# Optimization experiments

Hardware: AMD Instinct MI355X
Metric: run time of the kernel (lower is better)

The kernel has to match this reference:

```python
import jax, jax.numpy as jnp
import numpy as np
from jax import lax

N_LAYER = 24
N_EMBD = 1024
FFN = 4 * N_EMBD
LN_EPS = 1e-5


def setup_inputs() -> dict:
    key = jax.random.key(0)
    ks = jax.random.split(key, 24)
    L, C, F = N_LAYER, N_EMBD, FFN
    s = C ** -0.5  # keep GEMV outputs O(1) so exp() stays finite

    def rn(k, shape, scale=1.0):
        return jax.random.normal(k, shape, dtype=jnp.float32) * scale

    state = jnp.concatenate([
        rn(ks[1], (1, L, C)),                                          # statea: prev ln1 output
        rn(ks[2], (1, L, C), 0.1),                                     # stateb: wkv numerator acc
        jax.random.uniform(ks[3], (1, L, C), dtype=jnp.float32) + 0.5, # statec: wkv denominator acc (>0)
        rn(ks[4], (1, L, C)),                                          # stated: prev ln2 output
    ], axis=0)

    return {
        "x": rn(ks[0], (C,)),
        "state": state,
        "ln1w": 1.0 + rn(ks[5], (L, C), 0.02),
        "ln1b": rn(ks[6], (L, C), 0.02),
        "ln2w": 1.0 + rn(ks[7], (L, C), 0.02),
        "ln2b": rn(ks[8], (L, C), 0.02),
        "time_decay": -jnp.abs(rn(ks[9], (L, C))) - 0.1,
        "time_first": rn(ks[10], (L, C), 0.1),
        "kktk": jax.random.uniform(ks[11], (L, C), dtype=jnp.float32),
        "vvtv": jax.random.uniform(ks[12], (L, C), dtype=jnp.float32),
        "rrtr": jax.random.uniform(ks[13], (L, C), dtype=jnp.float32),
        "key": rn(ks[14], (L, 3, C, C), s),        # [kk, vv, -rr] stacks
        "outputv": rn(ks[15], (L, C, C), s),
        "time_mix_k_ffn": jax.random.uniform(ks[16], (L, C), dtype=jnp.float32),
        "time_mix_r_ffn": jax.random.uniform(ks[17], (L, C), dtype=jnp.float32),
        "key_ffn": rn(ks[18], (L, F, C), s),
        "receptance_ffn": rn(ks[19], (L, C, C), s),  # stored pre-negated, as in the module
        "value_ffn": rn(ks[20], (L, C, F), F ** -0.5),
    }


def _ln(v, w, b):
    m = v.mean()
    var = ((v - m) ** 2).mean()
    return (v - m) * lax.rsqrt(var + LN_EPS) * w + b


def reference(x, state, ln1w, ln1b, ln2w, ln2b, time_decay, time_first,
              kktk, vvtv, rrtr, key, outputv, time_mix_k_ffn, time_mix_r_ffn,
              key_ffn, receptance_ffn, value_ffn):
    # offset = 0, so the state slice covers all layers
    statea, stateb, statec, stated = state[0], state[1], state[2], state[3]  # each [L, C]
    # token-shift contributions precomputed against previous-step state
    kk_s = kktk * statea
    vv_s = vvtv * statea
    rr_s = rrtr * statea
    tmk_s = time_mix_k_ffn * stated
    tmr_s = time_mix_r_ffn * stated

    def layer(xc, p):
        (l1w, l1b, l2w, l2b, td, tfst, kks, vvs, rrs, keym, outv,
         tmk, tmr, kffn, rffn, vffn, sb, sc) = p
        xy = _ln(xc, l1w, l1b)
        k = keym[0] @ (xy + kks)
        v = keym[1] @ (xy + vvs)
        r = keym[2] @ (xy + rrs)   # keym[2] holds -receptance weights
        etfk = jnp.exp(tfst + k)
        w = (sb + etfk * v) / (sc * jnp.exp(r) + jnp.exp(tfst + k + r) + sc + etfk)
        sxx = xc + outv @ w
        ek = jnp.exp(k)
        ed = jnp.exp(td)
        sb_new = sb * ed + ek * v
        sc_new = sc * ed + ek
        xx = _ln(sxx, l2w, l2b)
        kf = jnp.square(jax.nn.relu(kffn @ (xx + tmk)))
        rf = jnp.exp(rffn @ (xx + tmr))  # rffn already negated
        x_new = sxx + (vffn @ kf) / (rf + 1.0)
        return x_new, (xy, sb_new, sc_new, xx)

    xs = (ln1w, ln1b, ln2w, ln2b, time_decay, time_first, kk_s, vv_s, rr_s,
          key, outputv, tmk_s, tmr_s, key_ffn, receptance_ffn, value_ffn,
          stateb, statec)
    x_out, (sa_n, sb_n, sc_n, sd_n) = lax.scan(layer, x, xs)
    new_state = jnp.stack([sa_n, sb_n, sc_n, sd_n])  # [4, L, C]
    return x_out, new_state
```

## Files before the change

kernel.cpp:

```cpp
#include <hip/hip_runtime.h>
#include <math.h>
#include <stddef.h>

#define NLAYER 24
#define NEMBD  1024
#define NFFN   4096
#define NB     256
#define NT     256
#define NW     4
#define LN_EPS 1e-5f

#define OUT_SA (NEMBD)
#define OUT_SB (NEMBD + NLAYER*NEMBD)
#define OUT_SC (NEMBD + 2*NLAYER*NEMBD)
#define OUT_SD (NEMBD + 3*NLAYER*NEMBD)

#define FLAG_STRIDE 32

struct Params {
  const float *x, *state, *ln1w, *ln1b, *ln2w, *ln2b, *td, *tf, *kktk, *vvtv, *rrtr;
  const float *key, *outputv, *tmk, *tmr, *kffn, *rffn, *vffn;
  float *out;
  float *xbuf, *kvr, *sxx, *rfb, *kfb;
  unsigned *flags;
};

__device__ __forceinline__ float wred(float v) {
#pragma unroll
  for (int o = 32; o > 0; o >>= 1) v += __shfl_xor(v, o, 64);
  return v;
}

__device__ __forceinline__ float dot4(float4 a, float4 b) {
  return a.x*b.x + a.y*b.y + a.z*b.z + a.w*b.w;
}

__device__ __forceinline__ float gload(const float* a) {
  return __hip_atomic_load(a, __ATOMIC_RELAXED, __HIP_MEMORY_SCOPE_AGENT);
}
__device__ __forceinline__ void gstore(float* a, float v) {
  __hip_atomic_store(a, v, __ATOMIC_RELAXED, __HIP_MEMORY_SCOPE_AGENT);
}

__device__ __forceinline__ void bar_arrive(unsigned* flags, unsigned tgt) {
  __syncthreads();
  asm volatile("" ::: "memory");
  if (threadIdx.x == 0) {
    __hip_atomic_store(&flags[(unsigned)blockIdx.x * FLAG_STRIDE], tgt,
                       __ATOMIC_RELAXED, __HIP_MEMORY_SCOPE_AGENT);
  }
  asm volatile("" ::: "memory");
}

__device__ __forceinline__ void bar_wait(unsigned* flags, unsigned tgt) {
  asm volatile("" ::: "memory");
  long spin = 0;
  while (__hip_atomic_load(&flags[(unsigned)threadIdx.x * FLAG_STRIDE],
                           __ATOMIC_RELAXED, __HIP_MEMORY_SCOPE_AGENT) < tgt) {
    __builtin_amdgcn_s_sleep(1);
    if (++spin > (1L << 18)) break;
  }
  asm volatile("" ::: "memory");
  __syncthreads();
}

__global__ void __launch_bounds__(NT, 1)
rwkv_persistent(Params p) {
  const int b    = blockIdx.x;
  const int t    = threadIdx.x;
  const int wid  = t >> 6;
  const int lane = t & 63;

  __shared__ float lds[NFFN];
  __shared__ float reda[NW], redq[NW];
  __shared__ float mrs[2];

  float4 wr[20];
  unsigned g = 1;

  {
    const float* W = p.key + (size_t)(b * 12 + wid * 3) * NEMBD + lane * 4;
#pragma unroll
    for (int r = 0; r < 3; ++r)
#pragma unroll
      for (int jj = 0; jj < 4; ++jj)
        wr[r * 4 + jj] = *(const float4*)&W[(size_t)r * NEMBD + jj * 256];
  }

  for (int l = 0; l < NLAYER; ++l) {
    {
      const int i0 = t * 4;
      float xa[4];
      if (l == 0) {
        float4 x4 = *(const float4*)&p.x[i0];
        xa[0] = x4.x; xa[1] = x4.y; xa[2] = x4.z; xa[3] = x4.w;
      } else {
#pragma unroll
        for (int j = 0; j < 4; ++j) xa[j] = gload(&p.xbuf[i0 + j]);
      }
      float s = xa[0] + xa[1] + xa[2] + xa[3];
      float q = xa[0]*xa[0] + xa[1]*xa[1] + xa[2]*xa[2] + xa[3]*xa[3];
      s = wred(s); q = wred(q);
      if (lane == 0) { reda[wid] = s; redq[wid] = q; }
      __syncthreads();
      if (t == 0) {
        float ts = 0.f, tq = 0.f;
#pragma unroll
        for (int i = 0; i < NW; ++i) { ts += reda[i]; tq += redq[i]; }
        float m = ts * (1.f / NEMBD);
        float var = tq * (1.f / NEMBD) - m * m;
        mrs[0] = m; mrs[1] = rsqrtf(var + LN_EPS);
      }
      __syncthreads();
      float m = mrs[0], rs = mrs[1];
      const float* l1w = p.ln1w + l * NEMBD;
      const float* l1b = p.ln1b + l * NEMBD;
      const float* sa  = p.state + 0 * NLAYER * NEMBD + l * NEMBD;
      const float* kkp = p.kktk + l * NEMBD;
      const float* vvp = p.vvtv + l * NEMBD;
      const float* rrp = p.rrtr + l * NEMBD;
#pragma unroll
      for (int j = 0; j < 4; ++j) {
        int i = i0 + j;
        float xy = (xa[j] - m) * rs * l1w[i] + l1b[i];
        float sav = sa[i];
        lds[i]             = xy + kkp[i] * sav;
        lds[NEMBD + i]     = xy + vvp[i] * sav;
        lds[2 * NEMBD + i] = xy + rrp[i] * sav;
        if (b == 0) p.out[OUT_SA + l * NEMBD + i] = xy;
      }
      __syncthreads();

      const int r0 = b * 12 + wid * 3;
      const float* v0 = lds + ((r0 + 0) >> 10) * NEMBD;
      const float* v1 = lds + ((r0 + 1) >> 10) * NEMBD;
      const float* v2 = lds + ((r0 + 2) >> 10) * NEMBD;
      float a0 = 0.f, a1 = 0.f, a2 = 0.f;
#pragma unroll
      for (int jj = 0; jj < 4; ++jj) {
        int col = lane * 4 + jj * 256;
        a0 += dot4(wr[0 * 4 + jj], *(const float4*)&v0[col]);
        a1 += dot4(wr[1 * 4 + jj], *(const float4*)&v1[col]);
        a2 += dot4(wr[2 * 4 + jj], *(const float4*)&v2[col]);
      }
      a0 = wred(a0); a1 = wred(a1); a2 = wred(a2);
      if (lane == 0) {
        gstore(&p.kvr[r0 + 0], a0);
        gstore(&p.kvr[r0 + 1], a1);
        gstore(&p.kvr[r0 + 2], a2);
      }
    }
    bar_arrive(p.flags, g);
    const int row2 = b * 4 + wid;
    {
      const float* W = p.outputv + ((size_t)l * NEMBD + row2) * NEMBD + lane * 4;
#pragma unroll
      for (int jj = 0; jj < 4; ++jj)
        wr[jj] = *(const float4*)&W[jj * 256];
    }
    bar_wait(p.flags, g); ++g;

    {
      const int i0 = t * 4;
      const float* tfp = p.tf + l * NEMBD;
      const float* sbp = p.state + 1 * NLAYER * NEMBD + l * NEMBD;
      const float* scp = p.state + 2 * NLAYER * NEMBD + l * NEMBD;
      const float* tdp = p.td + l * NEMBD;
#pragma unroll
      for (int j = 0; j < 4; ++j) {
        int i = i0 + j;
        float k = gload(&p.kvr[i]);
        float v = gload(&p.kvr[NEMBD + i]);
        float r = gload(&p.kvr[2 * NEMBD + i]);
        float sb = sbp[i], sc = scp[i];
        float etfk = expf(tfp[i] + k);
        float er   = expf(r);
        lds[i] = (sb + etfk * v) / ((sc + etfk) * (1.f + er));
        if (b == 0) {
          float ek = expf(k), ed = expf(tdp[i]);
          p.out[OUT_SB + l * NEMBD + i] = sb * ed + ek * v;
          p.out[OUT_SC + l * NEMBD + i] = sc * ed + ek;
        }
      }
      __syncthreads();
      float acc = 0.f;
#pragma unroll
      for (int jj = 0; jj < 4; ++jj) {
        int col = lane * 4 + jj * 256;
        acc += dot4(wr[jj], *(const float4*)&lds[col]);
      }
      acc = wred(acc);
      if (lane == 0) {
        float xc = (l == 0) ? p.x[row2] : gload(&p.xbuf[row2]);
        gstore(&p.sxx[row2], xc + acc);
      }
    }
    bar_arrive(p.flags, g);
    int isk3[5], rid3[5], voff3[5];
    {
#pragma unroll
      for (int sI = 0; sI < 5; ++sI) {
        int qI = wid * 5 + sI;
        const float* wp;
        if (qI < 16) {
          int row = b * 16 + qI;
          wp = p.kffn + ((size_t)l * NFFN + row) * NEMBD;
          isk3[sI] = 1; rid3[sI] = row; voff3[sI] = 0;
        } else {
          int row = b * 4 + (qI - 16);
          wp = p.rffn + ((size_t)l * NEMBD + row) * NEMBD;
          isk3[sI] = 0; rid3[sI] = row; voff3[sI] = NEMBD;
        }
        wp += lane * 4;
#pragma unroll
        for (int jj = 0; jj < 4; ++jj)
          wr[sI * 4 + jj] = *(const float4*)&wp[jj * 256];
      }
    }
    bar_wait(p.flags, g); ++g;

    {
      const int i0 = t * 4;
      float xa[4];
#pragma unroll
      for (int j = 0; j < 4; ++j) xa[j] = gload(&p.sxx[i0 + j]);
      float s = xa[0] + xa[1] + xa[2] + xa[3];
      float q = xa[0]*xa[0] + xa[1]*xa[1] + xa[2]*xa[2] + xa[3]*xa[3];
      s = wred(s); q = wred(q);
      if (lane == 0) { reda[wid] = s; redq[wid] = q; }
      __syncthreads();
      if (t == 0) {
        float ts = 0.f, tq = 0.f;
#pragma unroll
        for (int i = 0; i < NW; ++i) { ts += reda[i]; tq += redq[i]; }
        float m = ts * (1.f / NEMBD);
        float var = tq * (1.f / NEMBD) - m * m;
        mrs[0] = m; mrs[1] = rsqrtf(var + LN_EPS);
      }
      __syncthreads();
      float m = mrs[0], rs = mrs[1];
      const float* l2w = p.ln2w + l * NEMBD;
      const float* l2b = p.ln2b + l * NEMBD;
      const float* sdp = p.state + 3 * NLAYER * NEMBD + l * NEMBD;
      const float* tmkp = p.tmk + l * NEMBD;
      const float* tmrp = p.tmr + l * NEMBD;
#pragma unroll
      for (int j = 0; j < 4; ++j) {
        int i = i0 + j;
        float xx = (xa[j] - m) * rs * l2w[i] + l2b[i];
        float sdv = sdp[i];
        lds[i]         = xx + tmkp[i] * sdv;
        lds[NEMBD + i] = xx + tmrp[i] * sdv;
        if (b == 0) p.out[OUT_SD + l * NEMBD + i] = xx;
      }
      __syncthreads();

      float acc[5] = {0.f, 0.f, 0.f, 0.f, 0.f};
#pragma unroll
      for (int jj = 0; jj < 4; ++jj) {
        int col = lane * 4 + jj * 256;
#pragma unroll
        for (int sI = 0; sI < 5; ++sI)
          acc[sI] += dot4(wr[sI * 4 + jj], *(const float4*)&lds[voff3[sI] + col]);
      }
#pragma unroll
      for (int sI = 0; sI < 5; ++sI) {
        float r = wred(acc[sI]);
        if (lane == 0) {
          if (isk3[sI]) { float kv = fmaxf(r, 0.f); gstore(&p.kfb[rid3[sI]], kv * kv); }
          else          { gstore(&p.rfb[rid3[sI]], expf(r)); }
        }
      }
    }
    bar_arrive(p.flags, g);
    const int row4 = b * 4 + wid;
    {
      const float* W = p.vffn + ((size_t)l * NEMBD + row4) * NFFN + lane * 4;
#pragma unroll
      for (int jj = 0; jj < 16; ++jj)
        wr[jj] = *(const float4*)&W[jj * 256];
    }
    bar_wait(p.flags, g); ++g;

    {
#pragma unroll
      for (int pass = 0; pass < 4; ++pass) {
        int idx = pass * NEMBD + t * 4;
        float a0 = gload(&p.kfb[idx + 0]);
        float a1 = gload(&p.kfb[idx + 1]);
        float a2 = gload(&p.kfb[idx + 2]);
        float a3 = gload(&p.kfb[idx + 3]);
        *(float4*)&lds[idx] = make_float4(a0, a1, a2, a3);
      }
      __syncthreads();
      float accA = 0.f, accB = 0.f;
#pragma unroll
      for (int jj = 0; jj < 16; jj += 2) {
        int col = lane * 4 + jj * 256;
        accA += dot4(wr[jj],     *(const float4*)&lds[col]);
        accB += dot4(wr[jj + 1], *(const float4*)&lds[col + 256]);
      }
      float acc = wred(accA + accB);
      if (lane == 0) {
        float xn = gload(&p.sxx[row4]) + acc / (gload(&p.rfb[row4]) + 1.f);
        if (l == NLAYER - 1) p.out[row4] = xn;
        else                 gstore(&p.xbuf[row4], xn);
      }
    }
    bar_arrive(p.flags, g);
    if (l < NLAYER - 1) {
      const float* W = p.key + (size_t)(l + 1) * 3 * NEMBD * NEMBD
                     + (size_t)(b * 12 + wid * 3) * NEMBD + lane * 4;
#pragma unroll
      for (int r = 0; r < 3; ++r)
#pragma unroll
        for (int jj = 0; jj < 4; ++jj)
          wr[r * 4 + jj] = *(const float4*)&W[(size_t)r * NEMBD + jj * 256];
    }
    bar_wait(p.flags, g); ++g;
  }
}

__global__ void rwkv_init(unsigned* flags) {
  flags[threadIdx.x * FLAG_STRIDE] = 0u;
}

extern "C" void kernel_launch(void* const* d_in, const int* in_sizes, int n_in,
                              void* d_out, int out_size, void* d_ws, size_t ws_size,
                              hipStream_t stream) {
  Params p;
  p.x       = (const float*)d_in[0];
  p.state   = (const float*)d_in[1];
  p.ln1w    = (const float*)d_in[2];
  p.ln1b    = (const float*)d_in[3];
  p.ln2w    = (const float*)d_in[4];
  p.ln2b    = (const float*)d_in[5];
  p.td      = (const float*)d_in[6];
  p.tf      = (const float*)d_in[7];
  p.kktk    = (const float*)d_in[8];
  p.vvtv    = (const float*)d_in[9];
  p.rrtr    = (const float*)d_in[10];
  p.key     = (const float*)d_in[11];
  p.outputv = (const float*)d_in[12];
  p.tmk     = (const float*)d_in[13];
  p.tmr     = (const float*)d_in[14];
  p.kffn    = (const float*)d_in[15];
  p.rffn    = (const float*)d_in[16];
  p.vffn    = (const float*)d_in[17];
  p.out     = (float*)d_out;

  float* ws = (float*)d_ws;
  p.xbuf = ws;
  p.kvr  = ws + NEMBD;
  p.sxx  = ws + 4 * NEMBD;
  p.rfb  = ws + 5 * NEMBD;
  p.kfb  = ws + 6 * NEMBD;
  p.flags = (unsigned*)((char*)d_ws + 49152);

  rwkv_init<<<1, NB, 0, stream>>>(p.flags);
  rwkv_persistent<<<NB, NT, 0, stream>>>(p);
}
```

Before: 534.8 us.

## Add dedicated polling wavefront for grid barrier and skip final-layer barrier

```diff
diff --git a/kernel.cpp b/kernel.cpp
--- a/kernel.cpp
+++ b/kernel.cpp
@@ -6,8 +6,8 @@
 #define NEMBD  1024
 #define NFFN   4096
 #define NB     256
-#define NT     256
-#define NW     4
+#define NT     320
+#define NWC    4
 #define LN_EPS 1e-5f
 
 #define OUT_SA (NEMBD)
@@ -42,43 +42,63 @@
   __hip_atomic_store(a, v, __ATOMIC_RELAXED, __HIP_MEMORY_SCOPE_AGENT);
 }
 
-__device__ __forceinline__ void bar_arrive(unsigned* flags, unsigned tgt) {
+__device__ __forceinline__ void bar_flag(unsigned* flags, unsigned tgt) {
   __syncthreads();
-  asm volatile("" ::: "memory");
   if (threadIdx.x == 0) {
     __hip_atomic_store(&flags[(unsigned)blockIdx.x * FLAG_STRIDE], tgt,
                        __ATOMIC_RELAXED, __HIP_MEMORY_SCOPE_AGENT);
   }
-  asm volatile("" ::: "memory");
-}
-
-__device__ __forceinline__ void bar_wait(unsigned* flags, unsigned tgt) {
-  asm volatile("" ::: "memory");
-  long spin = 0;
-  while (__hip_atomic_load(&flags[(unsigned)threadIdx.x * FLAG_STRIDE],
-                           __ATOMIC_RELAXED, __HIP_MEMORY_SCOPE_AGENT) < tgt) {
-    __builtin_amdgcn_s_sleep(1);
-    if (++spin > (1L << 18)) break;
+}
+
+__device__ __forceinline__ void bar_spin(unsigned* flags, unsigned tgt, unsigned* genw) {
+  const int wid  = threadIdx.x >> 6;
+  const int lane = threadIdx.x & 63;
+  if (wid == NWC) {
+    long spin = 0;
+    for (;;) {
+      bool mine = true;
+#pragma unroll
+      for (int j = 0; j < 4; ++j) {
+        unsigned f = __hip_atomic_load(&flags[(unsigned)(lane * 4 + j) * FLAG_STRIDE],
+                                       __ATOMIC_RELAXED, __HIP_MEMORY_SCOPE_AGENT);
+        mine &= (f >= tgt);
+      }
+      if (__all(mine)) break;
+      __builtin_amdgcn_s_sleep(1);
+      if (++spin > (1L << 18)) break;
+    }
+    if (lane == 0) {
+      __hip_atomic_store(genw, tgt, __ATOMIC_RELAXED, __HIP_MEMORY_SCOPE_WORKGROUP);
+    }
+  } else {
+    long spin = 0;
+    while (__hip_atomic_load(genw, __ATOMIC_RELAXED, __HIP_MEMORY_SCOPE_WORKGROUP) < tgt) {
+      __builtin_amdgcn_s_sleep(1);
+      if (++spin > (1L << 20)) break;
+    }
   }
-  asm volatile("" ::: "memory");
-  __syncthreads();
-}
-
-__global__ void __launch_bounds__(NT, 1)
+}
+
+__global__ void __launch_bounds__(NT, 2)
 rwkv_persistent(Params p) {
   const int b    = blockIdx.x;
   const int t    = threadIdx.x;
   const int wid  = t >> 6;
   const int lane = t & 63;
+  const bool cw  = (wid < NWC);
 
   __shared__ float lds[NFFN];
-  __shared__ float reda[NW], redq[NW];
+  __shared__ float reda[NWC], redq[NWC];
   __shared__ float mrs[2];
+  __shared__ unsigned genw;
+
+  if (t == 0) genw = 0u;
+  __syncthreads();
 
   float4 wr[20];
   unsigned g = 1;
 
-  {
+  if (cw) {
     const float* W = p.key + (size_t)(b * 12 + wid * 3) * NEMBD + lane * 4;
 #pragma unroll
     for (int r = 0; r < 3; ++r)
@@ -90,114 +110,123 @@
   for (int l = 0; l < NLAYER; ++l) {
     {
       const int i0 = t * 4;
-      float xa[4];
-      if (l == 0) {
-        float4 x4 = *(const float4*)&p.x[i0];
-        xa[0] = x4.x; xa[1] = x4.y; xa[2] = x4.z; xa[3] = x4.w;
-      } else {
-#pragma unroll
-        for (int j = 0; j < 4; ++j) xa[j] = gload(&p.xbuf[i0 + j]);
-      }
-      float s = xa[0] + xa[1] + xa[2] + xa[3];
-      float q = xa[0]*xa[0] + xa[1]*xa[1] + xa[2]*xa[2] + xa[3]*xa[3];
-      s = wred(s); q = wred(q);
-      if (lane == 0) { reda[wid] = s; redq[wid] = q; }
+      float xa[4] = {0.f, 0.f, 0.f, 0.f};
+      if (cw) {
+        if (l == 0) {
+          float4 x4 = *(const float4*)&p.x[i0];
+          xa[0] = x4.x; xa[1] = x4.y; xa[2] = x4.z; xa[3] = x4.w;
+        } else {
+#pragma unroll
+          for (int j = 0; j < 4; ++j) xa[j] = gload(&p.xbuf[i0 + j]);
+        }
+        float s = xa[0] + xa[1] + xa[2] + xa[3];
+        float q = xa[0]*xa[0] + xa[1]*xa[1] + xa[2]*xa[2] + xa[3]*xa[3];
+        s = wred(s); q = wred(q);
+        if (lane == 0) { reda[wid] = s; redq[wid] = q; }
+      }
       __syncthreads();
       if (t == 0) {
         float ts = 0.f, tq = 0.f;
 #pragma unroll
-        for (int i = 0; i < NW; ++i) { ts += reda[i]; tq += redq[i]; }
+        for (int i = 0; i < NWC; ++i) { ts += reda[i]; tq += redq[i]; }
         float m = ts * (1.f / NEMBD);
         float var = tq * (1.f / NEMBD) - m * m;
         mrs[0] = m; mrs[1] = rsqrtf(var + LN_EPS);
       }
       __syncthreads();
-      float m = mrs[0], rs = mrs[1];
-      const float* l1w = p.ln1w + l * NEMBD;
-      const float* l1b = p.ln1b + l * NEMBD;
-      const float* sa  = p.state + 0 * NLAYER * NEMBD + l * NEMBD;
-      const float* kkp = p.kktk + l * NEMBD;
-      const float* vvp = p.vvtv + l * NEMBD;
-      const float* rrp = p.rrtr + l * NEMBD;
-#pragma unroll
-      for (int j = 0; j < 4; ++j) {
-        int i = i0 + j;
-        float xy = (xa[j] - m) * rs * l1w[i] + l1b[i];
-        float sav = sa[i];
-        lds[i]             = xy + kkp[i] * sav;
-        lds[NEMBD + i]     = xy + vvp[i] * sav;
-        lds[2 * NEMBD + i] = xy + rrp[i] * sav;
-        if (b == 0) p.out[OUT_SA + l * NEMBD + i] = xy;
-      }
-      __syncthreads();
-
-      const int r0 = b * 12 + wid * 3;
-      const float* v0 = lds + ((r0 + 0) >> 10) * NEMBD;
-      const float* v1 = lds + ((r0 + 1) >> 10) * NEMBD;
-      const float* v2 = lds + ((r0 + 2) >> 10) * NEMBD;
-      float a0 = 0.f, a1 = 0.f, a2 = 0.f;
-#pragma unroll
-      for (int jj = 0; jj < 4; ++jj) {
-        int col = lane * 4 + jj * 256;
-        a0 += dot4(wr[0 * 4 + jj], *(const float4*)&v0[col]);
-        a1 += dot4(wr[1 * 4 + jj], *(const float4*)&v1[col]);
-        a2 += dot4(wr[2 * 4 + jj], *(const float4*)&v2[col]);
-      }
-      a0 = wred(a0); a1 = wred(a1); a2 = wred(a2);
-      if (lane == 0) {
-        gstore(&p.kvr[r0 + 0], a0);
-        gstore(&p.kvr[r0 + 1], a1);
-        gstore(&p.kvr[r0 + 2], a2);
-      }
-    }
-    bar_arrive(p.flags, g);
+      if (cw) {
+        float m = mrs[0], rs = mrs[1];
+        const float* l1w = p.ln1w + l * NEMBD;
+        const float* l1b = p.ln1b + l * NEMBD;
+        const float* sa  = p.state + 0 * NLAYER * NEMBD + l * NEMBD;
+        const float* kkp = p.kktk + l * NEMBD;
+        const float* vvp = p.vvtv + l * NEMBD;
+        const float* rrp = p.rrtr + l * NEMBD;
+#pragma unroll
+        for (int j = 0; j < 4; ++j) {
+          int i = i0 + j;
+          float xy = (xa[j] - m) * rs * l1w[i] + l1b[i];
+          float sav = sa[i];
+          lds[i]             = xy + kkp[i] * sav;
+          lds[NEMBD + i]     = xy + vvp[i] * sav;
+          lds[2 * NEMBD + i] = xy + rrp[i] * sav;
+          if (b == 0) p.out[OUT_SA + l * NEMBD + i] = xy;
+        }
+      }
+      __syncthreads();
+      if (cw) {
+        const int r0 = b * 12 + wid * 3;
+        const float* v0 = lds + ((r0 + 0) >> 10) * NEMBD;
+        const float* v1 = lds + ((r0 + 1) >> 10) * NEMBD;
+        const float* v2 = lds + ((r0 + 2) >> 10) * NEMBD;
+        float a0 = 0.f, a1 = 0.f, a2 = 0.f;
+#pragma unroll
+        for (int jj = 0; jj < 4; ++jj) {
+          int col = lane * 4 + jj * 256;
+          a0 += dot4(wr[0 * 4 + jj], *(const float4*)&v0[col]);
+          a1 += dot4(wr[1 * 4 + jj], *(const float4*)&v1[col]);
+          a2 += dot4(wr[2 * 4 + jj], *(const float4*)&v2[col]);
+        }
+        a0 = wred(a0); a1 = wred(a1); a2 = wred(a2);
+        if (lane == 0) {
+          gstore(&p.kvr[r0 + 0], a0);
+          gstore(&p.kvr[r0 + 1], a1);
+          gstore(&p.kvr[r0 + 2], a2);
+        }
+      }
+    }
+    bar_flag(p.flags, g);
     const int row2 = b * 4 + wid;
-    {
+    if (cw) {
       const float* W = p.outputv + ((size_t)l * NEMBD + row2) * NEMBD + lane * 4;
 #pragma unroll
       for (int jj = 0; jj < 4; ++jj)
         wr[jj] = *(const float4*)&W[jj * 256];
     }
-    bar_wait(p.flags, g); ++g;
+    bar_spin(p.flags, g, &genw); ++g;
 
     {
       const int i0 = t * 4;
-      const float* tfp = p.tf + l * NEMBD;
-      const float* sbp = p.state + 1 * NLAYER * NEMBD + l * NEMBD;
-      const float* scp = p.state + 2 * NLAYER * NEMBD + l * NEMBD;
-      const float* tdp = p.td + l * NEMBD;
-#pragma unroll
-      for (int j = 0; j < 4; ++j) {
-        int i = i0 + j;
-        float k = gload(&p.kvr[i]);
-        float v = gload(&p.kvr[NEMBD + i]);
-        float r = gload(&p.kvr[2 * NEMBD + i]);
-        float sb = sbp[i], sc = scp[i];
-        float etfk = expf(tfp[i] + k);
-        float er   = expf(r);
-        lds[i] = (sb + etfk * v) / ((sc + etfk) * (1.f + er));
-        if (b == 0) {
-          float ek = expf(k), ed = expf(tdp[i]);
-          p.out[OUT_SB + l * NEMBD + i] = sb * ed + ek * v;
-          p.out[OUT_SC + l * NEMBD + i] = sc * ed + ek;
-        }
-      }
-      __syncthreads();
-      float acc = 0.f;
-#pragma unroll
-      for (int jj = 0; jj < 4; ++jj) {
-        int col = lane * 4 + jj * 256;
-        acc += dot4(wr[jj], *(const float4*)&lds[col]);
-      }
-      acc = wred(acc);
-      if (lane == 0) {
-        float xc = (l == 0) ? p.x[row2] : gload(&p.xbuf[row2]);
-        gstore(&p.sxx[row2], xc + acc);
-      }
-    }
-    bar_arrive(p.flags, g);
+      if (cw) {
+        const float* tfp = p.tf + l * NEMBD;
+        const float* sbp = p.state + 1 * NLAYER * NEMBD + l * NEMBD;
+        const float* scp = p.state + 2 * NLAYER * NEMBD + l * NEMBD;
+        const float* tdp = p.td + l * NEMBD;
+#pragma unroll
+        for (int j = 0; j < 4; ++j) {
+          int i = i0 + j;
+          float k = gload(&p.kvr[i]);
+          float v = gload(&p.kvr[NEMBD + i]);
+          float r = gload(&p.kvr[2 * NEMBD + i]);
+          float sb = sbp[i], sc = scp[i];
+          float etfk = expf(tfp[i] + k);
+          float er   = expf(r);
+          lds[i] = (sb + etfk * v) / ((sc + etfk) * (1.f + er));
+          if (b == 0) {
+            float ek = expf(k), ed = expf(tdp[i]);
+            p.out[OUT_SB + l * NEMBD + i] = sb * ed + ek * v;
+            p.out[OUT_SC + l * NEMBD + i] = sc * ed + ek;
+          }
+        }
+      }
+      __syncthreads();
+      if (cw) {
+        float acc = 0.f;
+#pragma unroll
+        for (int jj = 0; jj < 4; ++jj) {
+          int col = lane * 4 + jj * 256;
+          acc += dot4(wr[jj], *(const float4*)&lds[col]);
+        }
+        acc = wred(acc);
+        if (lane == 0) {
+          float xc = (l == 0) ? p.x[row2] : gload(&p.xbuf[row2]);
+          gstore(&p.sxx[row2], xc + acc);
+        }
+      }
+    }
+    bar_flag(p.flags, g);
     int isk3[5], rid3[5], voff3[5];
-    {
+    if (cw) {
 #pragma unroll
       for (int sI = 0; sI < 5; ++sI) {
         int qI = wid * 5 + sI;
@@ -217,107 +246,118 @@
           wr[sI * 4 + jj] = *(const float4*)&wp[jj * 256];
       }
     }
-    bar_wait(p.flags, g); ++g;
+    bar_spin(p.flags, g, &genw); ++g;
 
     {
       const int i0 = t * 4;
-      float xa[4];
-#pragma unroll
-      for (int j = 0; j < 4; ++j) xa[j] = gload(&p.sxx[i0 + j]);
-      float s = xa[0] + xa[1] + xa[2] + xa[3];
-      float q = xa[0]*xa[0] + xa[1]*xa[1] + xa[2]*xa[2] + xa[3]*xa[3];
-      s = wred(s); q = wred(q);
-      if (lane == 0) { reda[wid] = s; redq[wid] = q; }
+      float xa[4] = {0.f, 0.f, 0.f, 0.f};
+      if (cw) {
+#pragma unroll
+        for (int j = 0; j < 4; ++j) xa[j] = gload(&p.sxx[i0 + j]);
+        float s = xa[0] + xa[1] + xa[2] + xa[3];
+        float q = xa[0]*xa[0] + xa[1]*xa[1] + xa[2]*xa[2] + xa[3]*xa[3];
+        s = wred(s); q = wred(q);
+        if (lane == 0) { reda[wid] = s; redq[wid] = q; }
+      }
       __syncthreads();
       if (t == 0) {
         float ts = 0.f, tq = 0.f;
 #pragma unroll
-        for (int i = 0; i < NW; ++i) { ts += reda[i]; tq += redq[i]; }
+        for (int i = 0; i < NWC; ++i) { ts += reda[i]; tq += redq[i]; }
         float m = ts * (1.f / NEMBD);
         float var = tq * (1.f / NEMBD) - m * m;
         mrs[0] = m; mrs[1] = rsqrtf(var + LN_EPS);
       }
       __syncthreads();
-      float m = mrs[0], rs = mrs[1];
-      const float* l2w = p.ln2w + l * NEMBD;
-      const float* l2b = p.ln2b + l * NEMBD;
-      const float* sdp = p.state + 3 * NLAYER * NEMBD + l * NEMBD;
-      const float* tmkp = p.tmk + l * NEMBD;
-      const float* tmrp = p.tmr + l * NEMBD;
-#pragma unroll
-      for (int j = 0; j < 4; ++j) {
-        int i = i0 + j;
-        float xx = (xa[j] - m) * rs * l2w[i] + l2b[i];
-        float sdv = sdp[i];
-        lds[i]         = xx + tmkp[i] * sdv;
-        lds[NEMBD + i] = xx + tmrp[i] * sdv;
-        if (b == 0) p.out[OUT_SD + l * NEMBD + i] = xx;
-      }
-      __syncthreads();
-
-      float acc[5] = {0.f, 0.f, 0.f, 0.f, 0.f};
-#pragma unroll
-      for (int jj = 0; jj < 4; ++jj) {
-        int col = lane * 4 + jj * 256;
-#pragma unroll
-        for (int sI = 0; sI < 5; ++sI)
-          acc[sI] += dot4(wr[sI * 4 + jj], *(const float4*)&lds[voff3[sI] + col]);
-      }
-#pragma unroll
-      for (int sI = 0; sI < 5; ++sI) {
-        float r = wred(acc[sI]);
-        if (lane == 0) {
-          if (isk3[sI]) { float kv = fmaxf(r, 0.f); gstore(&p.kfb[rid3[sI]], kv * kv); }
-          else          { gstore(&p.rfb[rid3[sI]], expf(r)); }
-        }
-      }
-    }
-    bar_arrive(p.flags, g);
+      if (cw) {
+        float m = mrs[0], rs = mrs[1];
+        const float* l2w = p.ln2w + l * NEMBD;
+        const float* l2b = p.ln2b + l * NEMBD;
+        const float* sdp = p.state + 3 * NLAYER * NEMBD + l * NEMBD;
+        const float* tmkp = p.tmk + l * NEMBD;
+        const float* tmrp = p.tmr + l * NEMBD;
+#pragma unroll
+        for (int j = 0; j < 4; ++j) {
+          int i = i0 + j;
+          float xx = (xa[j] - m) * rs * l2w[i] + l2b[i];
+          float sdv = sdp[i];
+          lds[i]         = xx + tmkp[i] * sdv;
+          lds[NEMBD + i] = xx + tmrp[i] * sdv;
+          if (b == 0) p.out[OUT_SD + l * NEMBD + i] = xx;
+        }
+      }
+      __syncthreads();
+      if (cw) {
+        float acc[5] = {0.f, 0.f, 0.f, 0.f, 0.f};
+#pragma unroll
+        for (int jj = 0; jj < 4; ++jj) {
+          int col = lane * 4 + jj * 256;
+#pragma unroll
+          for (int sI = 0; sI < 5; ++sI)
+            acc[sI] += dot4(wr[sI * 4 + jj], *(const float4*)&lds[voff3[sI] + col]);
+        }
+#pragma unroll
+        for (int sI = 0; sI < 5; ++sI) {
+          float r = wred(acc[sI]);
+          if (lane == 0) {
+            if (isk3[sI]) { float kv = fmaxf(r, 0.f); gstore(&p.kfb[rid3[sI]], kv * kv); }
+            else          { gstore(&p.rfb[rid3[sI]], expf(r)); }
+          }
+        }
+      }
+    }
+    bar_flag(p.flags, g);
     const int row4 = b * 4 + wid;
-    {
+    if (cw) {
       const float* W = p.vffn + ((size_t)l * NEMBD + row4) * NFFN + lane * 4;
 #pragma unroll
       for (int jj = 0; jj < 16; ++jj)
         wr[jj] = *(const float4*)&W[jj * 256];
     }
-    bar_wait(p.flags, g); ++g;
+    bar_spin(p.flags, g, &genw); ++g;
 
     {
-#pragma unroll
-      for (int pass = 0; pass < 4; ++pass) {
-        int idx = pass * NEMBD + t * 4;
-        float a0 = gload(&p.kfb[idx + 0]);
-        float a1 = gload(&p.kfb[idx + 1]);
-        float a2 = gload(&p.kfb[idx + 2]);
-        float a3 = gload(&p.kfb[idx + 3]);
-        *(float4*)&lds[idx] = make_float4(a0, a1, a2, a3);
-      }
-      __syncthreads();
-      float accA = 0.f, accB = 0.f;
-#pragma unroll
-      for (int jj = 0; jj < 16; jj += 2) {
-        int col = lane * 4 + jj * 256;
-        accA += dot4(wr[jj],     *(const float4*)&lds[col]);
-        accB += dot4(wr[jj + 1], *(const float4*)&lds[col + 256]);
-      }
-      float acc = wred(accA + accB);
-      if (lane == 0) {
-        float xn = gload(&p.sxx[row4]) + acc / (gload(&p.rfb[row4]) + 1.f);
-        if (l == NLAYER - 1) p.out[row4] = xn;
-        else                 gstore(&p.xbuf[row4], xn);
-      }
-    }
-    bar_arrive(p.flags, g);
+      if (cw) {
+#pragma unroll
+        for (int pass = 0; pass < 4; ++pass) {
+          int idx = pass * NEMBD + t * 4;
+          float a0 = gload(&p.kfb[idx + 0]);
+          float a1 = gload(&p.kfb[idx + 1]);
+          float a2 = gload(&p.kfb[idx + 2]);
+          float a3 = gload(&p.kfb[idx + 3]);
+          *(float4*)&lds[idx] = make_float4(a0, a1, a2, a3);
+        }
+      }
+      __syncthreads();
+      if (cw) {
+        float accA = 0.f, accB = 0.f;
+#pragma unroll
+        for (int jj = 0; jj < 16; jj += 2) {
+          int col = lane * 4 + jj * 256;
+          accA += dot4(wr[jj],     *(const float4*)&lds[col]);
+          accB += dot4(wr[jj + 1], *(const float4*)&lds[col + 256]);
+        }
+        float acc = wred(accA + accB);
+        if (lane == 0) {
+          float xn = gload(&p.sxx[row4]) + acc / (gload(&p.rfb[row4]) + 1.f);
+          if (l == NLAYER - 1) p.out[row4] = xn;
+          else                 gstore(&p.xbuf[row4], xn);
+        }
+      }
+    }
     if (l < NLAYER - 1) {
-      const float* W = p.key + (size_t)(l + 1) * 3 * NEMBD * NEMBD
-                     + (size_t)(b * 12 + wid * 3) * NEMBD + lane * 4;
-#pragma unroll
-      for (int r = 0; r < 3; ++r)
-#pragma unroll
-        for (int jj = 0; jj < 4; ++jj)
-          wr[r * 4 + jj] = *(const float4*)&W[(size_t)r * NEMBD + jj * 256];
-    }
-    bar_wait(p.flags, g); ++g;
+      bar_flag(p.flags, g);
+      if (cw) {
+        const float* W = p.key + (size_t)(l + 1) * 3 * NEMBD * NEMBD
+                       + (size_t)(b * 12 + wid * 3) * NEMBD + lane * 4;
+#pragma unroll
+        for (int r = 0; r < 3; ++r)
+#pragma unroll
+          for (int jj = 0; jj < 4; ++jj)
+            wr[r * 4 + jj] = *(const float4*)&W[(size_t)r * NEMBD + jj * 256];
+      }
+      bar_spin(p.flags, g, &genw); ++g;
+    }
   }
 }
 
```

New measurement: 685.4 us. 1.28x slower.

## Dedicate an orchestrator wave to grid sync and stage inter-block data in LDS

Applied to the files above, without the earlier changes.

```diff
diff --git a/kernel.cpp b/kernel.cpp
--- a/kernel.cpp
+++ b/kernel.cpp
@@ -7,7 +7,6 @@
 #define NFFN   4096
 #define NB     256
 #define NT     256
-#define NW     4
 #define LN_EPS 1e-5f
 
 #define OUT_SA (NEMBD)
@@ -16,6 +15,17 @@
 #define OUT_SD (NEMBD + 3*NLAYER*NEMBD)
 
 #define FLAG_STRIDE 32
+
+#define LA    0
+#define LX    4096
+#define LB    5120
+#define LD    6144
+#define LE    9216
+#define LF    10240
+#define LRES  11264
+#define LRFB  11296
+#define LPART 11300
+#define LDS_FLOATS 11312
 
 struct Params {
   const float *x, *state, *ln1w, *ln1b, *ln2w, *ln2b, *td, *tf, *kktk, *vvtv, *rrtr;
@@ -30,11 +40,12 @@
   for (int o = 32; o > 0; o >>= 1) v += __shfl_xor(v, o, 64);
   return v;
 }
-
 __device__ __forceinline__ float dot4(float4 a, float4 b) {
   return a.x*b.x + a.y*b.y + a.z*b.z + a.w*b.w;
 }
-
+__device__ __forceinline__ float fcomp(float4 v, int j) {
+  return j == 0 ? v.x : (j == 1 ? v.y : (j == 2 ? v.z : v.w));
+}
 __device__ __forceinline__ float gload(const float* a) {
   return __hip_atomic_load(a, __ATOMIC_RELAXED, __HIP_MEMORY_SCOPE_AGENT);
 }
@@ -42,26 +53,11 @@
   __hip_atomic_store(a, v, __ATOMIC_RELAXED, __HIP_MEMORY_SCOPE_AGENT);
 }
 
-__device__ __forceinline__ void bar_arrive(unsigned* flags, unsigned tgt) {
-  __syncthreads();
-  asm volatile("" ::: "memory");
-  if (threadIdx.x == 0) {
-    __hip_atomic_store(&flags[(unsigned)blockIdx.x * FLAG_STRIDE], tgt,
-                       __ATOMIC_RELAXED, __HIP_MEMORY_SCOPE_AGENT);
-  }
-  asm volatile("" ::: "memory");
-}
-
-__device__ __forceinline__ void bar_wait(unsigned* flags, unsigned tgt) {
-  asm volatile("" ::: "memory");
-  long spin = 0;
-  while (__hip_atomic_load(&flags[(unsigned)threadIdx.x * FLAG_STRIDE],
-                           __ATOMIC_RELAXED, __HIP_MEMORY_SCOPE_AGENT) < tgt) {
-    __builtin_amdgcn_s_sleep(1);
-    if (++spin > (1L << 18)) break;
-  }
-  asm volatile("" ::: "memory");
-  __syncthreads();
+__device__ __forceinline__ void lbar() {
+  __builtin_amdgcn_sched_barrier(0);
+  asm volatile("s_waitcnt lgkmcnt(0)" ::: "memory");
+  __builtin_amdgcn_s_barrier();
+  __builtin_amdgcn_sched_barrier(0);
 }
 
 __global__ void __launch_bounds__(NT, 1)
@@ -70,254 +66,360 @@
   const int t    = threadIdx.x;
   const int wid  = t >> 6;
   const int lane = t & 63;
-
-  __shared__ float lds[NFFN];
-  __shared__ float reda[NW], redq[NW];
-  __shared__ float mrs[2];
-
-  float4 wr[20];
-  unsigned g = 1;
-
-  {
-    const float* W = p.key + (size_t)(b * 12 + wid * 3) * NEMBD + lane * 4;
-#pragma unroll
-    for (int r = 0; r < 3; ++r)
+  const bool orch = (wid == 0);
+  const int cw   = wid - 1;
+  const int i0   = t * 4;
+
+  __shared__ float sm[LDS_FLOATS];
+  __shared__ unsigned genw;
+  volatile unsigned* gw = &genw;
+
+  if (t == 0) genw = 0u;
+  __syncthreads();
+
+  float4 wr[28];
+  float4 pr[6];
+
+  auto load_pr1 = [&](int L) {
+    const int o = L * NEMBD + i0;
+    pr[0] = *(const float4*)&p.ln1w[o];
+    pr[1] = *(const float4*)&p.ln1b[o];
+    pr[2] = *(const float4*)&p.state[0 * NLAYER * NEMBD + o];
+    pr[3] = *(const float4*)&p.kktk[o];
+    pr[4] = *(const float4*)&p.vvtv[o];
+    pr[5] = *(const float4*)&p.rrtr[o];
+  };
+  auto load_pr2 = [&](int L) {
+    const int o = L * NEMBD + i0;
+    pr[0] = *(const float4*)&p.tf[o];
+    pr[1] = *(const float4*)&p.state[1 * NLAYER * NEMBD + o];
+    pr[2] = *(const float4*)&p.state[2 * NLAYER * NEMBD + o];
+    pr[3] = *(const float4*)&p.td[o];
+  };
+  auto load_pr3 = [&](int L) {
+    const int o = L * NEMBD + i0;
+    pr[0] = *(const float4*)&p.ln2w[o];
+    pr[1] = *(const float4*)&p.ln2b[o];
+    pr[2] = *(const float4*)&p.state[3 * NLAYER * NEMBD + o];
+    pr[3] = *(const float4*)&p.tmk[o];
+    pr[4] = *(const float4*)&p.tmr[o];
+  };
+  auto load_wr1 = [&](int L) {
+    const int r0 = b * 12 + cw * 4;
+    const float* W = p.key + (size_t)L * 3 * NEMBD * NEMBD + (size_t)r0 * NEMBD + lane * 4;
+#pragma unroll
+    for (int q = 0; q < 4; ++q)
 #pragma unroll
       for (int jj = 0; jj < 4; ++jj)
-        wr[r * 4 + jj] = *(const float4*)&W[(size_t)r * NEMBD + jj * 256];
+        wr[q * 4 + jj] = *(const float4*)&W[(size_t)q * NEMBD + jj * 256];
+  };
+  auto load_wr2 = [&](int L) {
+    const int nr = (cw == 0) ? 2 : 1;
+    const int rl0 = (cw == 0) ? 0 : (cw + 1);
+#pragma unroll
+    for (int r = 0; r < 2; ++r) if (r < nr) {
+      const float* W = p.outputv + ((size_t)L * NEMBD + b * 4 + rl0 + r) * NEMBD + lane * 4;
+#pragma unroll
+      for (int jj = 0; jj < 4; ++jj)
+        wr[r * 4 + jj] = *(const float4*)&W[jj * 256];
+    }
+  };
+  auto load_wr3 = [&](int L) {
+#pragma unroll
+    for (int e = 0; e < 7; ++e) {
+      const int sidx = cw * 7 + e;
+      if (sidx < 20) {
+        const float* W = (sidx < 16)
+          ? p.kffn + ((size_t)L * NFFN  + b * 16 + sidx) * NEMBD
+          : p.rffn + ((size_t)L * NEMBD + b * 4 + (sidx - 16)) * NEMBD;
+        W += lane * 4;
+#pragma unroll
+        for (int jj = 0; jj < 4; ++jj)
+          wr[e * 4 + jj] = *(const float4*)&W[jj * 256];
+      }
+    }
+  };
+  auto load_wr4 = [&](int L) {
+    const int jbase = (cw == 0) ? 0 : ((cw == 1) ? 6 : 11);
+    const int jn    = (cw == 0) ? 6 : 5;
+#pragma unroll
+    for (int r = 0; r < 4; ++r) {
+      const float* W = p.vffn + ((size_t)L * NEMBD + b * 4 + r) * NFFN + lane * 4;
+#pragma unroll
+      for (int c = 0; c < 6; ++c) if (c < jn)
+        wr[r * 6 + c] = *(const float4*)&W[(jbase + c) * 256];
+    }
+  };
+  auto ln_stats = [&](const float xa[4], float& m, float& rs) {
+    float s = xa[0] + xa[1] + xa[2] + xa[3];
+    float q = xa[0]*xa[0] + xa[1]*xa[1] + xa[2]*xa[2] + xa[3]*xa[3];
+    s = wred(s); q = wred(q);
+    if (lane == 0) { sm[LPART + wid] = s; sm[LPART + 4 + wid] = q; }
+    lbar();
+    float ts = sm[LPART+0] + sm[LPART+1] + sm[LPART+2] + sm[LPART+3];
+    float tq = sm[LPART+4] + sm[LPART+5] + sm[LPART+6] + sm[LPART+7];
+    m = ts * (1.f / NEMBD);
+    rs = rsqrtf(tq * (1.f / NEMBD) - m * m + LN_EPS);
+  };
+  auto spin_ge = [&](unsigned tgt) {
+    long c = 0;
+    while (*gw < tgt) { __builtin_amdgcn_s_sleep(1); if (++c > (1L << 20)) break; }
+    asm volatile("" ::: "memory");
+  };
+  auto flag_pub = [&](unsigned v) {
+    asm volatile("s_waitcnt vmcnt(0)" ::: "memory");
+    if (lane == 0)
+      __hip_atomic_store(&p.flags[(unsigned)b * FLAG_STRIDE], v,
+                         __ATOMIC_RELAXED, __HIP_MEMORY_SCOPE_AGENT);
+  };
+  auto poll = [&](unsigned v) {
+    long c = 0;
+    for (;;) {
+      bool mine = true;
+#pragma unroll
+      for (int j = 0; j < 4; ++j) {
+        unsigned f = __hip_atomic_load(&p.flags[(unsigned)(lane * 4 + j) * FLAG_STRIDE],
+                                       __ATOMIC_RELAXED, __HIP_MEMORY_SCOPE_AGENT);
+        mine &= (f >= v);
+      }
+      if (__all(mine)) break;
+      __builtin_amdgcn_s_sleep(1);
+      if (++c > (1L << 18)) break;
+    }
+  };
+  auto post_gen = [&](unsigned v) {
+    asm volatile("s_waitcnt lgkmcnt(0)" ::: "memory");
+    __builtin_amdgcn_sched_barrier(0);
+    if (lane == 0) *gw = v;
+  };
+
+  if (orch) {
+#pragma unroll
+    for (int c = 0; c < 4; ++c)
+      *(float4*)&sm[LX + lane * 4 + c * 256] = *(const float4*)&p.x[lane * 4 + c * 256];
+    load_pr1(0);
+    post_gen(1u);
+  } else {
+    load_pr1(0); load_wr1(0);
   }
 
   for (int l = 0; l < NLAYER; ++l) {
+    const bool w1 = (b == (l * 4 + 0) % NB);
+    const bool w2 = (b == (l * 4 + 1) % NB);
+    const bool w3 = (b == (l * 4 + 2) % NB);
+
     {
-      const int i0 = t * 4;
-      float xa[4];
-      if (l == 0) {
-        float4 x4 = *(const float4*)&p.x[i0];
-        xa[0] = x4.x; xa[1] = x4.y; xa[2] = x4.z; xa[3] = x4.w;
-      } else {
-#pragma unroll
-        for (int j = 0; j < 4; ++j) xa[j] = gload(&p.xbuf[i0 + j]);
-      }
-      float s = xa[0] + xa[1] + xa[2] + xa[3];
-      float q = xa[0]*xa[0] + xa[1]*xa[1] + xa[2]*xa[2] + xa[3]*xa[3];
-      s = wred(s); q = wred(q);
-      if (lane == 0) { reda[wid] = s; redq[wid] = q; }
-      __syncthreads();
-      if (t == 0) {
-        float ts = 0.f, tq = 0.f;
-#pragma unroll
-        for (int i = 0; i < NW; ++i) { ts += reda[i]; tq += redq[i]; }
-        float m = ts * (1.f / NEMBD);
-        float var = tq * (1.f / NEMBD) - m * m;
-        mrs[0] = m; mrs[1] = rsqrtf(var + LN_EPS);
-      }
-      __syncthreads();
-      float m = mrs[0], rs = mrs[1];
-      const float* l1w = p.ln1w + l * NEMBD;
-      const float* l1b = p.ln1b + l * NEMBD;
-      const float* sa  = p.state + 0 * NLAYER * NEMBD + l * NEMBD;
-      const float* kkp = p.kktk + l * NEMBD;
-      const float* vvp = p.vvtv + l * NEMBD;
-      const float* rrp = p.rrtr + l * NEMBD;
+      const unsigned s = (unsigned)(l * 4 + 1);
+      if (!orch) spin_ge(s);
+      float4 xv = *(const float4*)&sm[LX + i0];
+      float xa[4] = {xv.x, xv.y, xv.z, xv.w};
+      float m, rs; ln_stats(xa, m, rs);
 #pragma unroll
       for (int j = 0; j < 4; ++j) {
         int i = i0 + j;
-        float xy = (xa[j] - m) * rs * l1w[i] + l1b[i];
-        float sav = sa[i];
-        lds[i]             = xy + kkp[i] * sav;
-        lds[NEMBD + i]     = xy + vvp[i] * sav;
-        lds[2 * NEMBD + i] = xy + rrp[i] * sav;
-        if (b == 0) p.out[OUT_SA + l * NEMBD + i] = xy;
-      }
-      __syncthreads();
-
-      const int r0 = b * 12 + wid * 3;
-      const float* v0 = lds + ((r0 + 0) >> 10) * NEMBD;
-      const float* v1 = lds + ((r0 + 1) >> 10) * NEMBD;
-      const float* v2 = lds + ((r0 + 2) >> 10) * NEMBD;
-      float a0 = 0.f, a1 = 0.f, a2 = 0.f;
-#pragma unroll
-      for (int jj = 0; jj < 4; ++jj) {
-        int col = lane * 4 + jj * 256;
-        a0 += dot4(wr[0 * 4 + jj], *(const float4*)&v0[col]);
-        a1 += dot4(wr[1 * 4 + jj], *(const float4*)&v1[col]);
-        a2 += dot4(wr[2 * 4 + jj], *(const float4*)&v2[col]);
-      }
-      a0 = wred(a0); a1 = wred(a1); a2 = wred(a2);
-      if (lane == 0) {
-        gstore(&p.kvr[r0 + 0], a0);
-        gstore(&p.kvr[r0 + 1], a1);
-        gstore(&p.kvr[r0 + 2], a2);
-      }
-    }
-    bar_arrive(p.flags, g);
-    const int row2 = b * 4 + wid;
+        float xy  = (xa[j] - m) * rs * fcomp(pr[0], j) + fcomp(pr[1], j);
+        float sav = fcomp(pr[2], j);
+        sm[LD + i]        = xy + fcomp(pr[3], j) * sav;
+        sm[LD + 1024 + i] = xy + fcomp(pr[4], j) * sav;
+        sm[LD + 2048 + i] = xy + fcomp(pr[5], j) * sav;
+        if (w1) sm[LE + i] = xy;
+      }
+      lbar();
+      if (!orch) {
+        const int r0 = b * 12 + cw * 4;
+        const int mb = LD + (r0 >> 10) * 1024;
+#pragma unroll
+        for (int q = 0; q < 4; ++q) {
+          float a = 0.f;
+#pragma unroll
+          for (int jj = 0; jj < 4; ++jj)
+            a += dot4(wr[q * 4 + jj], *(const float4*)&sm[mb + lane * 4 + jj * 256]);
+          a = wred(a);
+          if (lane == 0) sm[LRES + cw * 4 + q] = a;
+        }
+        load_pr2(l); load_wr2(l);
+      }
+      lbar();
+      if (orch) {
+        if (lane < 12) gstore(&p.kvr[b * 12 + lane], sm[LRES + lane]);
+        flag_pub(s);
+        if (w1) {
+#pragma unroll
+          for (int c = 0; c < 4; ++c)
+            *(float4*)&p.out[OUT_SA + l * NEMBD + lane * 4 + c * 256] =
+              *(float4*)&sm[LE + lane * 4 + c * 256];
+        }
+        poll(s);
+#pragma unroll
+        for (int c = 0; c < 12; ++c) {
+          const int o = lane * 4 + c * 256;
+          *(float4*)&sm[LA + o] = make_float4(gload(&p.kvr[o]), gload(&p.kvr[o+1]),
+                                              gload(&p.kvr[o+2]), gload(&p.kvr[o+3]));
+        }
+        load_pr2(l);
+        post_gen(s + 1);
+      }
+    }
+
     {
-      const float* W = p.outputv + ((size_t)l * NEMBD + row2) * NEMBD + lane * 4;
-#pragma unroll
-      for (int jj = 0; jj < 4; ++jj)
-        wr[jj] = *(const float4*)&W[jj * 256];
-    }
-    bar_wait(p.flags, g); ++g;
+      const unsigned s = (unsigned)(l * 4 + 2);
+      if (!orch) spin_ge(s);
+      float4 kv = *(const float4*)&sm[LA + i0];
+      float4 vv = *(const float4*)&sm[LA + 1024 + i0];
+      float4 rv = *(const float4*)&sm[LA + 2048 + i0];
+#pragma unroll
+      for (int j = 0; j < 4; ++j) {
+        float k = fcomp(kv, j), v = fcomp(vv, j), r = fcomp(rv, j);
+        float tf = fcomp(pr[0], j), sb = fcomp(pr[1], j), sc = fcomp(pr[2], j);
+        float etfk = expf(tf + k);
+        float er   = expf(r);
+        sm[LD + i0 + j] = (sb + etfk * v) / ((sc + etfk) * (1.f + er));
+        if (w2) {
+          float ek = expf(k), ed = expf(fcomp(pr[3], j));
+          sm[LE + i0 + j] = sb * ed + ek * v;
+          sm[LF + i0 + j] = sc * ed + ek;
+        }
+      }
+      lbar();
+      if (!orch) {
+        const int nr = (cw == 0) ? 2 : 1;
+        const int rl0 = (cw == 0) ? 0 : (cw + 1);
+#pragma unroll
+        for (int r = 0; r < 2; ++r) if (r < nr) {
+          float a = 0.f;
+#pragma unroll
+          for (int jj = 0; jj < 4; ++jj)
+            a += dot4(wr[r * 4 + jj], *(const float4*)&sm[LD + lane * 4 + jj * 256]);
+          a = wred(a);
+          if (lane == 0) sm[LRES + rl0 + r] = a;
+        }
+        load_pr3(l); load_wr3(l);
+      }
+      lbar();
+      if (orch) {
+        if (lane < 4)
+          gstore(&p.sxx[b * 4 + lane], sm[LX + b * 4 + lane] + sm[LRES + lane]);
+        flag_pub(s);
+        if (w2) {
+#pragma unroll
+          for (int c = 0; c < 4; ++c) {
+            const int o = lane * 4 + c * 256;
+            *(float4*)&p.out[OUT_SB + l * NEMBD + o] = *(float4*)&sm[LE + o];
+            *(float4*)&p.out[OUT_SC + l * NEMBD + o] = *(float4*)&sm[LF + o];
+          }
+        }
+        poll(s);
+#pragma unroll
+        for (int c = 0; c < 4; ++c) {
+          const int o = lane * 4 + c * 256;
+          *(float4*)&sm[LB + o] = make_float4(gload(&p.sxx[o]), gload(&p.sxx[o+1]),
+                                              gload(&p.sxx[o+2]), gload(&p.sxx[o+3]));
+        }
+        load_pr3(l);
+        post_gen(s + 1);
+      }
+    }
 
     {
-      const int i0 = t * 4;
-      const float* tfp = p.tf + l * NEMBD;
-      const float* sbp = p.state + 1 * NLAYER * NEMBD + l * NEMBD;
-      const float* scp = p.state + 2 * NLAYER * NEMBD + l * NEMBD;
-      const float* tdp = p.td + l * NEMBD;
+      const unsigned s = (unsigned)(l * 4 + 3);
+      if (!orch) spin_ge(s);
+      float4 xv = *(const float4*)&sm[LB + i0];
+      float xa[4] = {xv.x, xv.y, xv.z, xv.w};
+      float m, rs; ln_stats(xa, m, rs);
 #pragma unroll
       for (int j = 0; j < 4; ++j) {
         int i = i0 + j;
-        float k = gload(&p.kvr[i]);
-        float v = gload(&p.kvr[NEMBD + i]);
-        float r = gload(&p.kvr[2 * NEMBD + i]);
-        float sb = sbp[i], sc = scp[i];
-        float etfk = expf(tfp[i] + k);
-        float er   = expf(r);
-        lds[i] = (sb + etfk * v) / ((sc + etfk) * (1.f + er));
-        if (b == 0) {
-          float ek = expf(k), ed = expf(tdp[i]);
-          p.out[OUT_SB + l * NEMBD + i] = sb * ed + ek * v;
-          p.out[OUT_SC + l * NEMBD + i] = sc * ed + ek;
-        }
-      }
-      __syncthreads();
-      float acc = 0.f;
-#pragma unroll
-      for (int jj = 0; jj < 4; ++jj) {
-        int col = lane * 4 + jj * 256;
-        acc += dot4(wr[jj], *(const float4*)&lds[col]);
-      }
-      acc = wred(acc);
-      if (lane == 0) {
-        float xc = (l == 0) ? p.x[row2] : gload(&p.xbuf[row2]);
-        gstore(&p.sxx[row2], xc + acc);
-      }
-    }
-    bar_arrive(p.flags, g);
-    int isk3[5], rid3[5], voff3[5];
+        float xx  = (xa[j] - m) * rs * fcomp(pr[0], j) + fcomp(pr[1], j);
+        float sdv = fcomp(pr[2], j);
+        sm[LD + i]        = xx + fcomp(pr[3], j) * sdv;
+        sm[LD + 1024 + i] = xx + fcomp(pr[4], j) * sdv;
+        if (w3) sm[LE + i] = xx;
+      }
+      lbar();
+      if (!orch) {
+#pragma unroll
+        for (int e = 0; e < 7; ++e) {
+          const int sidx = cw * 7 + e;
+          if (sidx < 20) {
+            const int mb = (sidx < 16) ? LD : LD + 1024;
+            float a = 0.f;
+#pragma unroll
+            for (int jj = 0; jj < 4; ++jj)
+              a += dot4(wr[e * 4 + jj], *(const float4*)&sm[mb + lane * 4 + jj * 256]);
+            a = wred(a);
+            if (lane == 0) {
+              if (sidx < 16) { float kk = fmaxf(a, 0.f); sm[LRES + sidx] = kk * kk; }
+              else { float ex = expf(a); sm[LRES + 16 + (sidx - 16)] = ex; sm[LRFB + (sidx - 16)] = ex; }
+            }
+          }
+        }
+        load_wr4(l);
+      }
+      lbar();
+      if (orch) {
+        if (lane < 16) gstore(&p.kfb[b * 16 + lane], sm[LRES + lane]);
+        if (lane < 4)  gstore(&p.rfb[b * 4 + lane],  sm[LRES + 16 + lane]);
+        flag_pub(s);
+        if (w3) {
+#pragma unroll
+          for (int c = 0; c < 4; ++c)
+            *(float4*)&p.out[OUT_SD + l * NEMBD + lane * 4 + c * 256] =
+              *(float4*)&sm[LE + lane * 4 + c * 256];
+        }
+        poll(s);
+#pragma unroll
+        for (int c = 0; c < 16; ++c) {
+          const int o = lane * 4 + c * 256;
+          *(float4*)&sm[LA + o] = make_float4(gload(&p.kfb[o]), gload(&p.kfb[o+1]),
+                                              gload(&p.kfb[o+2]), gload(&p.kfb[o+3]));
+        }
+        post_gen(s + 1);
+      }
+    }
+
     {
-#pragma unroll
-      for (int sI = 0; sI < 5; ++sI) {
-        int qI = wid * 5 + sI;
-        const float* wp;
-        if (qI < 16) {
-          int row = b * 16 + qI;
-          wp = p.kffn + ((size_t)l * NFFN + row) * NEMBD;
-          isk3[sI] = 1; rid3[sI] = row; voff3[sI] = 0;
+      const unsigned s = (unsigned)(l * 4 + 4);
+      if (!orch) {
+        spin_ge(s);
+        const int jbase = (cw == 0) ? 0 : ((cw == 1) ? 6 : 11);
+        const int jn    = (cw == 0) ? 6 : 5;
+#pragma unroll
+        for (int r = 0; r < 4; ++r) {
+          float a = 0.f;
+#pragma unroll
+          for (int c = 0; c < 6; ++c) if (c < jn)
+            a += dot4(wr[r * 6 + c], *(const float4*)&sm[LA + lane * 4 + (jbase + c) * 256]);
+          a = wred(a);
+          if (lane == 0) sm[LRES + r * 3 + cw] = a;
+        }
+        if (l < NLAYER - 1) { load_pr1(l + 1); load_wr1(l + 1); }
+      }
+      lbar();
+      if (orch) {
+        if (l == NLAYER - 1) {
+          if (lane < 4) {
+            float tot = sm[LRES + lane*3] + sm[LRES + lane*3 + 1] + sm[LRES + lane*3 + 2];
+            p.out[b * 4 + lane] = sm[LB + b * 4 + lane] + tot / (sm[LRFB + lane] + 1.f);
+          }
         } else {
-          int row = b * 4 + (qI - 16);
-          wp = p.rffn + ((size_t)l * NEMBD + row) * NEMBD;
-          isk3[sI] = 0; rid3[sI] = row; voff3[sI] = NEMBD;
-        }
-        wp += lane * 4;
-#pragma unroll
-        for (int jj = 0; jj < 4; ++jj)
-          wr[sI * 4 + jj] = *(const float4*)&wp[jj * 256];
-      }
-    }
-    bar_wait(p.flags, g); ++g;
-
-    {
-      const int i0 = t * 4;
-      float xa[4];
-#pragma unroll
-      for (int j = 0; j < 4; ++j) xa[j] = gload(&p.sxx[i0 + j]);
-      float s = xa[0] + xa[1] + xa[2] + xa[3];
-      float q = xa[0]*xa[0] + xa[1]*xa[1] + xa[2]*xa[2] + xa[3]*xa[3];
-      s = wred(s); q = wred(q);
-      if (lane == 0) { reda[wid] = s; redq[wid] = q; }
-      __syncthreads();
-      if (t == 0) {
-        float ts = 0.f, tq = 0.f;
-#pragma unroll
-        for (int i = 0; i < NW; ++i) { ts += reda[i]; tq += redq[i]; }
-        float m = ts * (1.f / NEMBD);
-        float var = tq * (1.f / NEMBD) - m * m;
-        mrs[0] = m; mrs[1] = rsqrtf(var + LN_EPS);
-      }
-      __syncthreads();
-      float m = mrs[0], rs = mrs[1];
-      const float* l2w = p.ln2w + l * NEMBD;
-      const float* l2b = p.ln2b + l * NEMBD;
-      const float* sdp = p.state + 3 * NLAYER * NEMBD + l * NEMBD;
-      const float* tmkp = p.tmk + l * NEMBD;
-      const float* tmrp = p.tmr + l * NEMBD;
-#pragma unroll
-      for (int j = 0; j < 4; ++j) {
-        int i = i0 + j;
-        float xx = (xa[j] - m) * rs * l2w[i] + l2b[i];
-        float sdv = sdp[i];
-        lds[i]         = xx + tmkp[i] * sdv;
-        lds[NEMBD + i] = xx + tmrp[i] * sdv;
-        if (b == 0) p.out[OUT_SD + l * NEMBD + i] = xx;
-      }
-      __syncthreads();
-
-      float acc[5] = {0.f, 0.f, 0.f, 0.f, 0.f};
-#pragma unroll
-      for (int jj = 0; jj < 4; ++jj) {
-        int col = lane * 4 + jj * 256;
-#pragma unroll
-        for (int sI = 0; sI < 5; ++sI)
-          acc[sI] += dot4(wr[sI * 4 + jj], *(const float4*)&lds[voff3[sI] + col]);
-      }
-#pragma unroll
-      for (int sI = 0; sI < 5; ++sI) {
-        float r = wred(acc[sI]);
-        if (lane == 0) {
-          if (isk3[sI]) { float kv = fmaxf(r, 0.f); gstore(&p.kfb[rid3[sI]], kv * kv); }
-          else          { gstore(&p.rfb[rid3[sI]], expf(r)); }
-        }
-      }
-    }
-    bar_arrive(p.flags, g);
-    const int row4 = b * 4 + wid;
-    {
-      const float* W = p.vffn + ((size_t)l * NEMBD + row4) * NFFN + lane * 4;
-#pragma unroll
-      for (int jj = 0; jj < 16; ++jj)
-        wr[jj] = *(const float4*)&W[jj * 256];
-    }
-    bar_wait(p.flags, g); ++g;
-
-    {
-#pragma unroll
-      for (int pass = 0; pass < 4; ++pass) {
-        int idx = pass * NEMBD + t * 4;
-        float a0 = gload(&p.kfb[idx + 0]);
-        float a1 = gload(&p.kfb[idx + 1]);
-        float a2 = gload(&p.kfb[idx + 2]);
-        float a3 = gload(&p.kfb[idx + 3]);
-        *(float4*)&lds[idx] = make_float4(a0, a1, a2, a3);
-      }
-      __syncthreads();
-      float accA = 0.f, accB = 0.f;
-#pragma unroll
-      for (int jj = 0; jj < 16; jj += 2) {
-        int col = lane * 4 + jj * 256;
-        accA += dot4(wr[jj],     *(const float4*)&lds[col]);
-        accB += dot4(wr[jj + 1], *(const float4*)&lds[col + 256]);
-      }
-      float acc = wred(accA + accB);
-      if (lane == 0) {
-        float xn = gload(&p.sxx[row4]) + acc / (gload(&p.rfb[row4]) + 1.f);
-        if (l == NLAYER - 1) p.out[row4] = xn;
-        else                 gstore(&p.xbuf[row4], xn);
-      }
-    }
-    bar_arrive(p.flags, g);
-    if (l < NLAYER - 1) {
-      const float* W = p.key + (size_t)(l + 1) * 3 * NEMBD * NEMBD
-                     + (size_t)(b * 12 + wid * 3) * NEMBD + lane * 4;
-#pragma unroll
-      for (int r = 0; r < 3; ++r)
-#pragma unroll
-        for (int jj = 0; jj < 4; ++jj)
-          wr[r * 4 + jj] = *(const float4*)&W[(size_t)r * NEMBD + jj * 256];
-    }
-    bar_wait(p.flags, g); ++g;
+          if (lane < 4) {
+            float tot = sm[LRES + lane*3] + sm[LRES + lane*3 + 1] + sm[LRES + lane*3 + 2];
+            float xn = sm[LB + b * 4 + lane] + tot / (sm[LRFB + lane] + 1.f);
+            gstore(&p.xbuf[b * 4 + lane], xn);
+          }
+          flag_pub(s);
+          poll(s);
+#pragma unroll
+          for (int c = 0; c < 4; ++c) {
+            const int o = lane * 4 + c * 256;
+            *(float4*)&sm[LX + o] = make_float4(gload(&p.xbuf[o]), gload(&p.xbuf[o+1]),
+                                                gload(&p.xbuf[o+2]), gload(&p.xbuf[o+3]));
+          }
+          load_pr1(l + 1);
+          post_gen(s + 1);
+        }
+      }
+    }
   }
 }
 
```

After: 860.7 us. 1.61x slower.
